# Optimization experiments

Hardware: AMD Instinct MI355X
Metric: run time of the kernel (lower is better)

Reference implementation:

```python
import jax, jax.numpy as jnp
import numpy as np

N = 8192
E = 262144
DIN = 512
DOUT = 256


def setup_inputs() -> dict:
    key = jax.random.key(0)
    k1, k2, k3, k4 = jax.random.split(key, 4)
    x = jax.random.normal(k1, (N, DIN), dtype=jnp.float32)
    edge_index = jax.random.randint(k2, (2, E), 0, N, dtype=jnp.int64)
    edge_weight = jax.random.uniform(k3, (E,), dtype=jnp.float32)
    W = jax.random.normal(k4, (DOUT, DIN), dtype=jnp.float32) * (1.0 / np.sqrt(DIN))
    return {"x": x, "edge_index": edge_index, "edge_weight": edge_weight, "W": W}


def reference(x, edge_index, edge_weight, W):
    n = x.shape[0]
    # Linear(dim_in, dim_out, bias=False): h = x @ W.T  -> [N, DOUT]
    h = x @ W.T
    # Dense adjacency: A[src, dst] += w (to_dense_adj sums duplicate edges)
    src, dst = edge_index[0], edge_index[1]
    A = jnp.zeros((n, n), dtype=x.dtype).at[src, dst].add(edge_weight)
    # degree from A BEFORE self-loops, then +1 from the added eye on degree_matrix
    deg = jnp.sum(A, axis=1) + 1.0
    # sqrt(inverse(diag(deg))) == diag(1/sqrt(deg)); apply as row scaling
    dinv_sqrt = 1.0 / jnp.sqrt(deg)  # [N]
    A = A + jnp.eye(n, dtype=x.dtype)  # self-loops on adjacency
    # x = D^{-1/2} @ (A.T @ (D^{-1/2} @ h))
    h = dinv_sqrt[:, None] * h
    h = A.T @ h
    h = dinv_sqrt[:, None] * h
    return h
```

## Files before the change

### kernel.cpp

```cpp
#include <hip/hip_runtime.h>

static constexpr int DIN = 512;
static constexpr int DOUT = 256;
static constexpr int CAP = 128;

typedef __attribute__((ext_vector_type(8))) short short8;
typedef __attribute__((ext_vector_type(4))) float f32x4;
typedef __attribute__((ext_vector_type(2))) unsigned int u32x2;
typedef __attribute__((ext_vector_type(4))) unsigned int u32x4;

__device__ inline unsigned short f2bf(float f) {
  unsigned int b = __float_as_uint(f);
  unsigned int r = (b + 0x7fffu + ((b >> 16) & 1u)) >> 16;
  return (unsigned short)r;
}
__device__ inline float bf_lo(unsigned int packed) { return __uint_as_float(packed << 16); }
__device__ inline float bf_hi(unsigned int packed) { return __uint_as_float(packed & 0xffff0000u); }

__device__ inline short8 cvt8(const f32x4 a, const f32x4 b) {
  short8 o;
  o[0] = (short)f2bf(a[0]); o[1] = (short)f2bf(a[1]);
  o[2] = (short)f2bf(a[2]); o[3] = (short)f2bf(a[3]);
  o[4] = (short)f2bf(b[0]); o[5] = (short)f2bf(b[1]);
  o[6] = (short)f2bf(b[2]); o[7] = (short)f2bf(b[3]);
  return o;
}

__global__ __launch_bounds__(256) void k_edges(
    const int* __restrict__ ei, const float* __restrict__ ew,
    const float* __restrict__ W,
    float* __restrict__ deg, int* __restrict__ cursor,
    uint2* __restrict__ bucket, unsigned short* __restrict__ wbb,
    int E, int EB) {
  const int b = blockIdx.x;
  if (b < EB) {
    int e = b * 256 + threadIdx.x;
    if (e < E) {
      int srcv = __builtin_nontemporal_load(ei + e);
      int dstv = __builtin_nontemporal_load(ei + E + e);
      float w = __builtin_nontemporal_load(ew + e);
      atomicAdd(&deg[srcv], w);
      int pos = atomicAdd(&cursor[dstv], 1);
      if (pos < CAP) {
        uint2 v;
        v.x = (unsigned)srcv;
        v.y = __float_as_uint(w);
        bucket[(size_t)dstv * CAP + pos] = v;
      }
    }
  } else {
    long i = (long)(b - EB) * 256 + threadIdx.x;
    const f32x4* src = (const f32x4*)(W + i * 8);
    f32x4 a = src[0], bb = src[1];
    *(short8*)(wbb + i * 8) = cvt8(a, bb);
  }
}

__global__ __launch_bounds__(256) void k_gemm_mfma(
    const float* __restrict__ x, const unsigned short* __restrict__ wbb,
    const float* __restrict__ deg, unsigned short* __restrict__ h1b) {
  const int lane = threadIdx.x & 63;
  const int wv = threadIdx.x >> 6;
  const int bm = blockIdx.x * 16;
  const int colb = wv * 64;
  const int r = lane & 15;
  const int kg = lane >> 4;
  f32x4 acc[4] = {};
  const float* arow = x + (size_t)(bm + r) * DIN + kg * 8;
  const unsigned short* brow0 = wbb + (size_t)(colb + r) * DIN + kg * 8;
#pragma unroll
  for (int k0 = 0; k0 < DIN; k0 += 32) {
    f32x4 a0 = __builtin_nontemporal_load((const f32x4*)(arow + k0));
    f32x4 a1 = __builtin_nontemporal_load((const f32x4*)(arow + k0 + 4));
    short8 av = cvt8(a0, a1);
#pragma unroll
    for (int nt = 0; nt < 4; ++nt) {
      short8 bv = *(const short8*)(brow0 + (size_t)nt * 16 * DIN + k0);
      acc[nt] = __builtin_amdgcn_mfma_f32_16x16x32_bf16(av, bv, acc[nt], 0, 0, 0);
    }
  }
#pragma unroll
  for (int i = 0; i < 4; ++i) {
    int row = bm + kg * 4 + i;
    float sr = __frsqrt_rn(1.0f + deg[row]);
#pragma unroll
    for (int nt = 0; nt < 4; ++nt) {
      h1b[(size_t)row * DOUT + colb + nt * 16 + r] = f2bf(sr * acc[nt][i]);
    }
  }
}

__global__ __launch_bounds__(256, 4) void k_gather(
    const unsigned short* __restrict__ h1b, const float* __restrict__ deg,
    const int* __restrict__ cursor, const uint2* __restrict__ bucket,
    float* __restrict__ out) {
  const int lane = threadIdx.x & 63;
  const int wv = threadIdx.x >> 6;
  const int dst = blockIdx.x * 4 + wv;
  const int cl = lane & 31;
  const int half = lane >> 5;
  const int cnt = min(cursor[dst], CAP);

  const u32x4 selfv = *(const u32x4*)(h1b + (size_t)dst * DOUT + cl * 8);
  const float sd = __frsqrt_rn(1.0f + deg[dst]);

  float acc[8] = {};

  for (int base = 0; base < cnt; base += 64) {
    const int c = min(64, cnt - base);
    int sv = 0;
    float wl = 0.f;
    if (lane < c) {
      u32x2 ev = __builtin_nontemporal_load(
          (const u32x2*)(bucket + (size_t)dst * CAP + base + lane));
      sv = (int)ev[0];
      wl = __uint_as_float(ev[1]);
    }
    const int npair = ((c + 15) >> 4) << 3;
    for (int j = 0; j < npair; j += 8) {
      u32x4 rbuf[8];
#pragma unroll
      for (int u = 0; u < 8; ++u) {
        int src = __shfl(sv, 2 * (j + u) + half);
        rbuf[u] = *(const u32x4*)(h1b + (size_t)src * DOUT + cl * 8);
      }
#pragma unroll
      for (int u = 0; u < 8; ++u) {
        float w = __shfl(wl, 2 * (j + u) + half);
        acc[0] = fmaf(w, bf_lo(rbuf[u][0]), acc[0]);
        acc[1] = fmaf(w, bf_hi(rbuf[u][0]), acc[1]);
        acc[2] = fmaf(w, bf_lo(rbuf[u][1]), acc[2]);
        acc[3] = fmaf(w, bf_hi(rbuf[u][1]), acc[3]);
        acc[4] = fmaf(w, bf_lo(rbuf[u][2]), acc[4]);
        acc[5] = fmaf(w, bf_hi(rbuf[u][2]), acc[5]);
        acc[6] = fmaf(w, bf_lo(rbuf[u][3]), acc[6]);
        acc[7] = fmaf(w, bf_hi(rbuf[u][3]), acc[7]);
      }
    }
  }

#pragma unroll
  for (int k = 0; k < 8; ++k) acc[k] += __shfl_xor(acc[k], 32);

  if (half == 0) {
    f32x4 o0v, o1v;
    o0v[0] = sd * (bf_lo(selfv[0]) + acc[0]);
    o0v[1] = sd * (bf_hi(selfv[0]) + acc[1]);
    o0v[2] = sd * (bf_lo(selfv[1]) + acc[2]);
    o0v[3] = sd * (bf_hi(selfv[1]) + acc[3]);
    o1v[0] = sd * (bf_lo(selfv[2]) + acc[4]);
    o1v[1] = sd * (bf_hi(selfv[2]) + acc[5]);
    o1v[2] = sd * (bf_lo(selfv[3]) + acc[6]);
    o1v[3] = sd * (bf_hi(selfv[3]) + acc[7]);
    float* op = out + (size_t)dst * DOUT + cl * 8;
    __builtin_nontemporal_store(o0v, (f32x4*)op);
    __builtin_nontemporal_store(o1v, (f32x4*)(op + 4));
  }
}

extern "C" void kernel_launch(void* const* d_in, const int* in_sizes, int n_in,
                              void* d_out, int out_size, void* d_ws, size_t ws_size,
                              hipStream_t stream) {
  const float* x = (const float*)d_in[0];
  const int* ei = (const int*)d_in[1];
  const float* ew = (const float*)d_in[2];
  const float* W = (const float*)d_in[3];
  float* out = (float*)d_out;

  const int n = in_sizes[0] / DIN;
  const int E = in_sizes[2];

  char* p = (char*)d_ws;
  auto alloc = [&](size_t bytes) {
    char* q = p;
    p += (bytes + 255) & ~(size_t)255;
    return q;
  };
  unsigned short* h1b = (unsigned short*)alloc((size_t)n * DOUT * 2);
  unsigned short* wbb = (unsigned short*)alloc((size_t)DOUT * DIN * 2);
  float* deg   = (float*)alloc((size_t)n * 4 * 2);
  int* cursor  = (int*)(deg + n);
  uint2* bucket = (uint2*)alloc((size_t)n * CAP * 8);

  const int EB = (E + 255) / 256;
  const int WB = (DOUT * DIN / 8 + 255) / 256;

  (void)hipMemsetAsync(deg, 0, (size_t)n * 8, stream);
  k_edges<<<EB + WB, 256, 0, stream>>>(ei, ew, W, deg, cursor, bucket, wbb, E, EB);
  k_gemm_mfma<<<n / 16, 256, 0, stream>>>(x, wbb, deg, h1b);
  k_gather<<<n / 4, 256, 0, stream>>>(h1b, deg, cursor, bucket, out);
}
```

Measured before the change: 76.65 us.

## Fuse edge bucketing with GEMM and move degree scaling into gather

Result: faster. 73.34 us (-4.3%).

```diff
diff --git a/kernel.cpp b/kernel.cpp
--- a/kernel.cpp
+++ b/kernel.cpp
@@ -26,15 +26,26 @@
   return o;
 }
 
-__global__ __launch_bounds__(256) void k_edges(
+__global__ __launch_bounds__(256) void k_prep(
+    const float* __restrict__ W, unsigned short* __restrict__ wbb,
+    int* __restrict__ dz, int n2, int wgroups) {
+  const int gid = blockIdx.x * 256 + threadIdx.x;
+  if (gid < n2) dz[gid] = 0;
+  const int wi = gid - n2;
+  if (wi >= 0 && wi < wgroups) {
+    const f32x4* src = (const f32x4*)(W + (size_t)wi * 8);
+    f32x4 a = src[0], b = src[1];
+    *(short8*)(wbb + (size_t)wi * 8) = cvt8(a, b);
+  }
+}
+
+__global__ __launch_bounds__(256) void k_fused(
     const int* __restrict__ ei, const float* __restrict__ ew,
-    const float* __restrict__ W,
+    const float* __restrict__ x, const unsigned short* __restrict__ wbb,
     float* __restrict__ deg, int* __restrict__ cursor,
-    uint2* __restrict__ bucket, unsigned short* __restrict__ wbb,
-    int E, int EB) {
-  const int b = blockIdx.x;
-  if (b < EB) {
-    int e = b * 256 + threadIdx.x;
+    uint2* __restrict__ bucket, unsigned short* __restrict__ h1b, int E) {
+  {
+    const int e = blockIdx.x * 256 + threadIdx.x;
     if (e < E) {
       int srcv = __builtin_nontemporal_load(ei + e);
       int dstv = __builtin_nontemporal_load(ei + E + e);
@@ -48,45 +59,31 @@
         bucket[(size_t)dstv * CAP + pos] = v;
       }
     }
-  } else {
-    long i = (long)(b - EB) * 256 + threadIdx.x;
-    const f32x4* src = (const f32x4*)(W + i * 8);
-    f32x4 a = src[0], bb = src[1];
-    *(short8*)(wbb + i * 8) = cvt8(a, bb);
   }
-}
-
-__global__ __launch_bounds__(256) void k_gemm_mfma(
-    const float* __restrict__ x, const unsigned short* __restrict__ wbb,
-    const float* __restrict__ deg, unsigned short* __restrict__ h1b) {
   const int lane = threadIdx.x & 63;
   const int wv = threadIdx.x >> 6;
-  const int bm = blockIdx.x * 16;
-  const int colb = wv * 64;
+  const int bm = (blockIdx.x >> 1) * 16;
+  const int colb = (blockIdx.x & 1) * 128 + wv * 32;
   const int r = lane & 15;
   const int kg = lane >> 4;
-  f32x4 acc[4] = {};
+  f32x4 acc[2] = {};
   const float* arow = x + (size_t)(bm + r) * DIN + kg * 8;
-  const unsigned short* brow0 = wbb + (size_t)(colb + r) * DIN + kg * 8;
+  const unsigned short* brow = wbb + (size_t)(colb + r) * DIN + kg * 8;
 #pragma unroll
   for (int k0 = 0; k0 < DIN; k0 += 32) {
-    f32x4 a0 = __builtin_nontemporal_load((const f32x4*)(arow + k0));
-    f32x4 a1 = __builtin_nontemporal_load((const f32x4*)(arow + k0 + 4));
+    f32x4 a0 = *(const f32x4*)(arow + k0);
+    f32x4 a1 = *(const f32x4*)(arow + k0 + 4);
     short8 av = cvt8(a0, a1);
-#pragma unroll
-    for (int nt = 0; nt < 4; ++nt) {
-      short8 bv = *(const short8*)(brow0 + (size_t)nt * 16 * DIN + k0);
-      acc[nt] = __builtin_amdgcn_mfma_f32_16x16x32_bf16(av, bv, acc[nt], 0, 0, 0);
-    }
+    short8 b0 = *(const short8*)(brow + k0);
+    short8 b1 = *(const short8*)(brow + (size_t)16 * DIN + k0);
+    acc[0] = __builtin_amdgcn_mfma_f32_16x16x32_bf16(av, b0, acc[0], 0, 0, 0);
+    acc[1] = __builtin_amdgcn_mfma_f32_16x16x32_bf16(av, b1, acc[1], 0, 0, 0);
   }
 #pragma unroll
   for (int i = 0; i < 4; ++i) {
     int row = bm + kg * 4 + i;
-    float sr = __frsqrt_rn(1.0f + deg[row]);
-#pragma unroll
-    for (int nt = 0; nt < 4; ++nt) {
-      h1b[(size_t)row * DOUT + colb + nt * 16 + r] = f2bf(sr * acc[nt][i]);
-    }
+    h1b[(size_t)row * DOUT + colb + r] = f2bf(acc[0][i]);
+    h1b[(size_t)row * DOUT + colb + 16 + r] = f2bf(acc[1][i]);
   }
 }
 
@@ -114,7 +111,7 @@
       u32x2 ev = __builtin_nontemporal_load(
           (const u32x2*)(bucket + (size_t)dst * CAP + base + lane));
       sv = (int)ev[0];
-      wl = __uint_as_float(ev[1]);
+      wl = __uint_as_float(ev[1]) * __frsqrt_rn(1.0f + deg[sv]);
     }
     const int npair = ((c + 15) >> 4) << 3;
     for (int j = 0; j < npair; j += 8) {
@@ -144,14 +141,14 @@
 
   if (half == 0) {
     f32x4 o0v, o1v;
-    o0v[0] = sd * (bf_lo(selfv[0]) + acc[0]);
-    o0v[1] = sd * (bf_hi(selfv[0]) + acc[1]);
-    o0v[2] = sd * (bf_lo(selfv[1]) + acc[2]);
-    o0v[3] = sd * (bf_hi(selfv[1]) + acc[3]);
-    o1v[0] = sd * (bf_lo(selfv[2]) + acc[4]);
-    o1v[1] = sd * (bf_hi(selfv[2]) + acc[5]);
-    o1v[2] = sd * (bf_lo(selfv[3]) + acc[6]);
-    o1v[3] = sd * (bf_hi(selfv[3]) + acc[7]);
+    o0v[0] = sd * fmaf(sd, bf_lo(selfv[0]), acc[0]);
+    o0v[1] = sd * fmaf(sd, bf_hi(selfv[0]), acc[1]);
+    o0v[2] = sd * fmaf(sd, bf_lo(selfv[1]), acc[2]);
+    o0v[3] = sd * fmaf(sd, bf_hi(selfv[1]), acc[3]);
+    o1v[0] = sd * fmaf(sd, bf_lo(selfv[2]), acc[4]);
+    o1v[1] = sd * fmaf(sd, bf_hi(selfv[2]), acc[5]);
+    o1v[2] = sd * fmaf(sd, bf_lo(selfv[3]), acc[6]);
+    o1v[3] = sd * fmaf(sd, bf_hi(selfv[3]), acc[7]);
     float* op = out + (size_t)dst * DOUT + cl * 8;
     __builtin_nontemporal_store(o0v, (f32x4*)op);
     __builtin_nontemporal_store(o1v, (f32x4*)(op + 4));
@@ -182,11 +179,12 @@
   int* cursor  = (int*)(deg + n);
   uint2* bucket = (uint2*)alloc((size_t)n * CAP * 8);
 
-  const int EB = (E + 255) / 256;
-  const int WB = (DOUT * DIN / 8 + 255) / 256;
+  const int n2 = 2 * n;
+  const int wgroups = DOUT * DIN / 8;
+  const int prep_blocks = (n2 + wgroups + 255) / 256;
 
-  (void)hipMemsetAsync(deg, 0, (size_t)n * 8, stream);
-  k_edges<<<EB + WB, 256, 0, stream>>>(ei, ew, W, deg, cursor, bucket, wbb, E, EB);
-  k_gemm_mfma<<<n / 16, 256, 0, stream>>>(x, wbb, deg, h1b);
+  k_prep<<<prep_blocks, 256, 0, stream>>>(W, wbb, (int*)deg, n2, wgroups);
+  k_fused<<<(E + 255) / 256, 256, 0, stream>>>(ei, ew, x, wbb, deg, cursor,
+                                               bucket, h1b, E);
   k_gather<<<n / 4, 256, 0, stream>>>(h1b, deg, cursor, bucket, out);
 }
```
